# Kernel optimization log

Measured on AMD Instinct MI355X. Metric: run time of the kernel, lower is better.

The kernel has to match this reference:

```python
import jax, jax.numpy as jnp
import numpy as np

B, N, D = 8, 1024, 768
H = 12
HD = D // H
LN_EPS = 1e-5
EPS = 1e-8


def setup_inputs() -> dict:
    key = jax.random.key(0)
    ks = jax.random.split(key, 16)
    s = 0.02
    return {
        "x": jax.random.normal(ks[0], (B, N, D), jnp.float32),
        "low_freq_feat": jax.random.normal(ks[1], (B, N, D), jnp.float32),
        "high_freq_feat": jax.random.normal(ks[2], (B, N, D), jnp.float32),
        "W_qkv_id": jax.random.normal(ks[3], (D, 3 * D), jnp.float32) * s,
        "W_qkv_attr": jax.random.normal(ks[4], (D, 3 * D), jnp.float32) * s,
        "W_fg_id": jax.random.normal(ks[5], (D, D), jnp.float32) * s,
        "b_fg_id": jnp.zeros((D,), jnp.float32),
        "W_fg_attr": jax.random.normal(ks[6], (D, D), jnp.float32) * s,
        "b_fg_attr": jnp.zeros((D,), jnp.float32),
        "W_proj_id": jax.random.normal(ks[7], (D, D), jnp.float32) * s,
        "b_proj_id": jnp.zeros((D,), jnp.float32),
        "W_proj_attr": jax.random.normal(ks[8], (D, D), jnp.float32) * s,
        "b_proj_attr": jnp.zeros((D,), jnp.float32),
        "ln_id_g": jnp.ones((D,), jnp.float32),
        "ln_id_b": jnp.zeros((D,), jnp.float32),
        "ln_attr_g": jnp.ones((D,), jnp.float32),
        "ln_attr_b": jnp.zeros((D,), jnp.float32),
        "ortho_temperature": jnp.float32(1.0),
        "freq_guide_strength": jnp.float32(0.3),
    }


def _layernorm(x, g, b):
    mu = x.mean(-1, keepdims=True)
    var = ((x - mu) ** 2).mean(-1, keepdims=True)
    return (x - mu) * jax.lax.rsqrt(var + LN_EPS) * g + b


def reference(x, low_freq_feat, high_freq_feat,
              W_qkv_id, W_qkv_attr,
              W_fg_id, b_fg_id, W_fg_attr, b_fg_attr,
              W_proj_id, b_proj_id, W_proj_attr, b_proj_attr,
              ln_id_g, ln_id_b, ln_attr_g, ln_attr_b,
              ortho_temperature, freq_guide_strength):
    b, n, d = x.shape
    scale = HD ** -0.5

    def split_qkv(t):
        t = t.reshape(b, n, 3, H, HD).transpose(2, 0, 3, 1, 4)
        return t[0], t[1], t[2]

    q_id, k_id, v_id = split_qkv(x @ W_qkv_id)
    q_at, k_at, v_at = split_qkv(x @ W_qkv_attr)

    fs = jax.nn.sigmoid(freq_guide_strength)
    low_g = (low_freq_feat @ W_fg_id + b_fg_id).reshape(b, n, H, HD).transpose(0, 2, 1, 3)
    high_g = (high_freq_feat @ W_fg_attr + b_fg_attr).reshape(b, n, H, HD).transpose(0, 2, 1, 3)
    v_id = v_id + fs * low_g
    v_at = v_at + fs * high_g

    def soft_attn(q, k):
        a = jnp.clip(jnp.einsum('bhnd,bhmd->bhnm', q, k) * scale, -20.0, 20.0)
        return jax.nn.softmax(a, axis=-1)

    attn_id = soft_attn(q_id, k_id)
    attn_at = soft_attn(q_at, k_at)

    # soft orthogonal mask (same mask for both branches)
    overlap = ((attn_id + EPS) * (attn_at + EPS)).sum(-1, keepdims=True)
    temp = jnp.clip(ortho_temperature, 0.1, 5.0)
    mask = jax.nn.sigmoid(-overlap * temp)

    def mask_renorm(a):
        m = a * mask
        m = m / (m.sum(-1, keepdims=True) + EPS)
        return jnp.where(jnp.isnan(m), jnp.zeros_like(m), m)

    attn_id = mask_renorm(attn_id)
    attn_at = mask_renorm(attn_at)

    def branch_out(a, v, W, bias, g, beta):
        o = jnp.einsum('bhnm,bhmd->bhnd', a, v).transpose(0, 2, 1, 3).reshape(b, n, d)
        return _layernorm(o @ W + bias, g, beta)

    id_features = branch_out(attn_id, v_id, W_proj_id, b_proj_id, ln_id_g, ln_id_b)
    attr_features = branch_out(attn_at, v_at, W_proj_attr, b_proj_attr, ln_attr_g, ln_attr_b)
    return (id_features, attr_features)
```

## Files before the change

### kernel.cpp

```cpp
#include <hip/hip_runtime.h>
#include <stdint.h>


typedef __attribute__((ext_vector_type(8))) _Float16 f16x8;
typedef __attribute__((ext_vector_type(4))) _Float16 f16x4;
typedef __attribute__((ext_vector_type(4))) float    f32x4;

__device__ __forceinline__ void g2l16(const void* g, void* l) {
  __builtin_amdgcn_global_load_lds(
      (const __attribute__((address_space(1))) void*)g,
      (__attribute__((address_space(3))) void*)l, 16, 0, 0);
}

#define BARX()   asm volatile("s_barrier" ::: "memory")
#define WAITV0() asm volatile("s_waitcnt vmcnt(0)" ::: "memory")
#define LGKM0()  asm volatile("s_waitcnt lgkmcnt(0)" ::: "memory")
#define SB0()    __builtin_amdgcn_sched_barrier(0)

#define MFMA12(NB)                                                            \
  __builtin_amdgcn_s_setprio(1);                                              \
  _Pragma("unroll")                                                           \
  for (int mt = 0; mt < 4; mt++)                                              \
    _Pragma("unroll")                                                         \
    for (int i = 0; i < 3; i++)                                               \
      acc[mt][(NB) + i] = SWAP                                                \
          ? __builtin_amdgcn_mfma_f32_16x16x32_f16(b[i], a[mt],               \
                                                   acc[mt][(NB) + i], 0, 0, 0)\
          : __builtin_amdgcn_mfma_f32_16x16x32_f16(a[mt], b[i],               \
                                                   acc[mt][(NB) + i], 0, 0, 0);\
  __builtin_amdgcn_s_setprio(0);

template <bool SWAP>
__device__ __forceinline__ void gemm192(const _Float16* __restrict__ A0,
                                        const _Float16* __restrict__ A1,
                                        const _Float16* __restrict__ B0,
                                        const _Float16* __restrict__ B1,
                                        int nb0, int nb1, int m0, int KT,
                                        _Float16* As, _Float16* Bs,
                                        f32x4 (&acc)[4][6]) {
  const int tid = threadIdx.x;
  const int lane = tid & 63, w = tid >> 6;
  const int wm = (w >> 1) * 64, wn = (w & 1) * 96;
  const int l15 = lane & 15, quad = lane >> 4;
  const int srow = lane >> 2;
  const int scol = ((lane & 3) ^ ((lane >> 3) & 3)) * 8;
  const int rg = (quad ^ ((l15 >> 1) & 3)) * 8;
  const int rdA = (wm + l15) * 32 + rg;
  const int rdB = (wn + l15) * 32 + rg;

  const _Float16* gA0a = A0 + (size_t)(m0 + (w * 2) * 16 + srow) * 768 + scol;
  const _Float16* gA1a = gA0a + (size_t)16 * 768;
  const _Float16* gA0b = A1 + (size_t)(m0 + (w * 2) * 16 + srow) * 768 + scol;
  const _Float16* gA1b = gA0b + (size_t)16 * 768;
  const _Float16* gBa[3]; const _Float16* gBb[3]; int lB[3];
#pragma unroll
  for (int i = 0; i < 3; i++) {
    int j = w * 3 + i, hb = j / 12, cb = j % 12;
    gBa[i] = B0 + (size_t)(nb0 + cb * 16 + srow) * 768 + hb * 32 + scol;
    gBb[i] = B1 + (size_t)(nb1 + cb * 16 + srow) * 768 + hb * 32 + scol;
    lB[i] = hb * 6144 + cb * 512;
  }

  auto stageA = [&](int t) {
    const bool s = t >= 12;
    const int kc = (s ? t - 12 : t) * 64;
    const _Float16* a0 = s ? gA0b : gA0a;
    const _Float16* a1 = s ? gA1b : gA1a;
    _Float16* Ab = As + (t & 1) * 16384 + w * 1024;
    g2l16(a0 + kc,      Ab);
    g2l16(a0 + kc + 32, Ab + 8192);
    g2l16(a1 + kc,      Ab + 512);
    g2l16(a1 + kc + 32, Ab + 8704);
  };
  auto stageB = [&](int t) {
    const bool s = t >= 12;
    const int kc = (s ? t - 12 : t) * 64;
    _Float16* Bb = Bs + (t & 1) * 12288;
#pragma unroll
    for (int i = 0; i < 3; i++) {
      const _Float16* p = s ? gBb[i] : gBa[i];
      g2l16(p + kc, Bb + lB[i]);
    }
  };

#pragma unroll
  for (int mt = 0; mt < 4; mt++)
#pragma unroll
    for (int nt = 0; nt < 6; nt++) acc[mt][nt] = (f32x4){0.f, 0.f, 0.f, 0.f};

  stageA(0); stageB(0);
  WAITV0();
  BARX();

  for (int t = 0; t < KT; t++) {
    const _Float16* as = As + (t & 1) * 16384;
    const _Float16* bs = Bs + (t & 1) * 12288;
    const bool st = (t + 1 < KT);
    f16x8 a[4], b[3];

#pragma unroll
    for (int mt = 0; mt < 4; mt++) a[mt] = *(const f16x8*)(as + rdA + mt * 512);
#pragma unroll
    for (int i = 0; i < 3; i++) b[i] = *(const f16x8*)(bs + rdB + i * 512);
    if (st) stageA(t + 1);
    BARX(); LGKM0(); SB0();
    MFMA12(0);
    SB0();
    BARX();

#pragma unroll
    for (int i = 0; i < 3; i++) b[i] = *(const f16x8*)(bs + rdB + (3 + i) * 512);
    if (st) stageB(t + 1);
    BARX(); LGKM0(); SB0();
    MFMA12(3);
    SB0();
    BARX();

#pragma unroll
    for (int mt = 0; mt < 4; mt++)
      a[mt] = *(const f16x8*)(as + 8192 + rdA + mt * 512);
#pragma unroll
    for (int i = 0; i < 3; i++)
      b[i] = *(const f16x8*)(bs + 6144 + rdB + i * 512);
    BARX(); LGKM0(); SB0();
    MFMA12(0);
    SB0();
    BARX();

#pragma unroll
    for (int i = 0; i < 3; i++)
      b[i] = *(const f16x8*)(bs + 6144 + rdB + (3 + i) * 512);
    BARX(); LGKM0(); SB0();
    MFMA12(3);
    SB0();
    WAITV0();
    BARX();
  }
}

__device__ __forceinline__ void tcast32(const float* __restrict__ src,
                                        _Float16* __restrict__ dst,
                                        int N, int n0, int k0) {
  __shared__ float t[32][33];
  int tr = threadIdx.x >> 5, tc = threadIdx.x & 31;
#pragma unroll
  for (int i = 0; i < 4; i++) {
    int r = tr + i * 8;
    t[r][tc] = src[(size_t)(k0 + r) * N + n0 + tc];
  }
  __syncthreads();
#pragma unroll
  for (int i = 0; i < 4; i++) {
    int r = tr + i * 8;
    dst[(size_t)(n0 + r) * 768 + k0 + tc] = (_Float16)t[tc][r];
  }
}

__global__ __launch_bounds__(256) void k_pre(const float* __restrict__ x,
                                             const float* __restrict__ lo,
                                             const float* __restrict__ hi,
                                             const float* __restrict__ fgs,
                                             const float* __restrict__ Wq0,
                                             const float* __restrict__ Wq1,
                                             const float* __restrict__ W0,
                                             const float* __restrict__ W1,
                                             const float* __restrict__ W2,
                                             const float* __restrict__ W3,
                                             _Float16* __restrict__ x_f,
                                             _Float16* __restrict__ low_f,
                                             _Float16* __restrict__ high_f,
                                             _Float16* __restrict__ Dq,
                                             _Float16* __restrict__ D0,
                                             _Float16* __restrict__ D1,
                                             _Float16* __restrict__ D2,
                                             _Float16* __restrict__ D3) {
  int blk = blockIdx.x;
  if (blk < 18432) {
    float scale = 1.f;
    const float* s; _Float16* d;
    if (blk < 6144)       { s = x;  d = x_f; }
    else if (blk < 12288) { s = lo; d = low_f;  blk -= 6144;
                            scale = 1.f / (1.f + __expf(-fgs[0])); }
    else                  { s = hi; d = high_f; blk -= 12288;
                            scale = 1.f / (1.f + __expf(-fgs[0])); }
    int i = blk * 256 + threadIdx.x;
    float4 v = ((const float4*)s)[i];
    f16x4 o = {(_Float16)(v.x * scale), (_Float16)(v.y * scale),
               (_Float16)(v.z * scale), (_Float16)(v.w * scale)};
    *(f16x4*)(d + (size_t)i * 4) = o;
    return;
  }
  blk -= 18432;
  if (blk < 3456) {
    int half = blk / 1728, rem = blk % 1728;
    int xx = rem % 72, yy = rem / 72;
    tcast32(half ? Wq1 : Wq0, Dq + (size_t)half * 2304 * 768, 2304, xx * 32, yy * 32);
  } else {
    blk -= 3456;
    int q = blk / 576, rem = blk % 576;
    int xx = rem % 24, yy = rem / 24;
    const float* src; _Float16* d;
    if (q == 0)      { src = W0; d = D0; }
    else if (q == 1) { src = W1; d = D1; }
    else if (q == 2) { src = W2; d = D2; }
    else             { src = W3; d = D3; }
    tcast32(src, d, 768, xx * 32, yy * 32);
  }
}

__global__ __launch_bounds__(512, 2) void k_gemm_qkv(const _Float16* __restrict__ x_f,
                                                     const _Float16* __restrict__ low_f,
                                                     const _Float16* __restrict__ high_f,
                                                     const _Float16* __restrict__ wqkvt,
                                                     const _Float16* __restrict__ wfgid,
                                                     const _Float16* __restrict__ wfgat,
                                                     const float* __restrict__ bfg_id,
                                                     const float* __restrict__ bfg_at,
                                                     const float* __restrict__ fgs,
                                                     _Float16* __restrict__ Qb,
                                                     _Float16* __restrict__ Kb,
                                                     _Float16* __restrict__ Vtb) {
  __shared__ alignas(16) _Float16 As[32768], Bs[24576];
  f32x4 acc[4][6];
  int bx = blockIdx.x, br = bx / 12, idx = bx % 12;
  int three = idx >> 2, sub = idx & 3;
  int m0 = blockIdx.y * 256;
  int n0abs = br * 2304 + three * 768 + sub * 192;
  int lane = threadIdx.x & 63, w = threadIdx.x >> 6;
  int wm = (w >> 1) * 64, wn = (w & 1) * 96, l15 = lane & 15, quad = lane >> 4;

  if (three == 2) {
    const _Float16* A1 = br ? high_f : low_f;
    const _Float16* B1 = br ? wfgat : wfgid;
    gemm192<false>(x_f, A1, wqkvt, B1, n0abs, sub * 192, m0, 24, As, Bs, acc);
    float fs = 1.f / (1.f + __expf(-fgs[0]));
    const float* bias = br ? bfg_at : bfg_id;
#pragma unroll
    for (int mt = 0; mt < 4; mt++)
#pragma unroll
      for (int nt = 0; nt < 6; nt++) {
        int c = sub * 192 + wn + nt * 16 + l15;
        int h = c >> 6, hd = c & 63;
        int m = m0 + wm + mt * 16 + quad * 4;
        int b = m >> 10, tok = m & 1023;
        size_t head = (size_t)(br * 96 + b * 12 + h);
        float bv = fs * bias[c];
        f32x4 v = acc[mt][nt];
        f16x4 o;
#pragma unroll
        for (int r = 0; r < 4; r++) o[r] = (_Float16)(v[r] + bv);
        *(f16x4*)(Vtb + (head * 64 + hd) * 1024 + tok) = o;
      }
  } else {
    gemm192<true>(x_f, x_f, wqkvt, wqkvt, n0abs, n0abs, m0, 12, As, Bs, acc);
    float qscl = (three == 0) ? 0.125f * 1.44269504f : 1.0f;
    _Float16* dst = (three == 0) ? Qb : Kb;
#pragma unroll
    for (int mt = 0; mt < 4; mt++)
#pragma unroll
      for (int nt = 0; nt < 6; nt++) {
        int m = m0 + wm + mt * 16 + l15;
        int c = sub * 192 + wn + nt * 16 + quad * 4;
        int h = c >> 6, hd = c & 63;
        int b = m >> 10, tok = m & 1023;
        size_t head = (size_t)(br * 96 + b * 12 + h);
        f32x4 v = acc[mt][nt];
        f16x4 o;
#pragma unroll
        for (int r = 0; r < 4; r++) o[r] = (_Float16)(v[r] * qscl);
        *(f16x4*)(dst + (head * 1024 + tok) * 64 + hd) = o;
      }
  }
}

__global__ __launch_bounds__(256, 3) void k_attn(const _Float16* __restrict__ Qb,
                                                 const _Float16* __restrict__ Kb,
                                                 const _Float16* __restrict__ Vtb,
                                                 _Float16* __restrict__ Ob) {
  __shared__ alignas(16) _Float16 Qs[128 * 64];
  __shared__ alignas(16) _Float16 Ks[128 * 64];
  __shared__ alignas(16) _Float16 Vts[64 * 128];
  int hl = blockIdx.x;
  int br = hl / 96, bh = hl % 96;
  int qbase = blockIdx.y * 128;
  const _Float16* Qh = Qb + (size_t)hl * 65536;
  const _Float16* Kh = Kb + (size_t)hl * 65536;
  const _Float16* Vth = Vtb + (size_t)hl * 65536;
  int lane = threadIdx.x & 63, w = threadIdx.x >> 6;
  int l15 = lane & 15, quad = lane >> 4;
  const int key7 = l15 & 7;

  {
    int rr = lane >> 3, sg = (lane & 7) ^ rr;
#pragma unroll
    for (int i = 0; i < 4; i++) {
      int c = w * 4 + i;
      g2l16(Qh + (size_t)(qbase + c * 8 + rr) * 64 + sg * 8, Qs + c * 512);
    }
  }
  auto stage_kv = [&](int n0) {
    int rr8 = lane >> 3, sg8 = ((lane & 7) ^ rr8) * 8;
    int rr16 = lane >> 4;
#pragma unroll
    for (int i = 0; i < 4; i++) {
      int c = w * 4 + i;
      g2l16(Kh + (size_t)(n0 + c * 8 + rr8) * 64 + sg8, Ks + c * 512);
      int vrow = c * 4 + rr16;
      int sg16 = ((lane & 15) ^ (vrow & 15)) * 8;
      g2l16(Vth + (size_t)vrow * 1024 + n0 + sg16, Vts + c * 512);
    }
  };
  stage_kv(0);

  f32x4 o[2][4];
#pragma unroll
  for (int qg = 0; qg < 2; qg++)
#pragma unroll
    for (int i = 0; i < 4; i++) o[qg][i] = (f32x4){0.f, 0.f, 0.f, 0.f};
  float rs0 = 0.f, rs1 = 0.f;
  f16x8 bq[2][2];
  const f32x4 zero = (f32x4){0.f, 0.f, 0.f, 0.f};
  const int g0 = (quad ^ key7) * 8, g1 = ((4 + quad) ^ key7) * 8;

  for (int kt = 0; kt < 8; kt++) {
    __syncthreads();
    if (kt == 0) {
#pragma unroll
      for (int qg = 0; qg < 2; qg++) {
        bq[qg][0] = *(const f16x8*)(Qs + (w * 32 + qg * 16 + l15) * 64 + g0);
        bq[qg][1] = *(const f16x8*)(Qs + (w * 32 + qg * 16 + l15) * 64 + g1);
      }
    }
    f32x4 c0, c1;
    {
      f16x8 a0 = *(const f16x8*)(Ks + l15 * 64 + g0);
      f16x8 a1 = *(const f16x8*)(Ks + l15 * 64 + g1);
      c0 = __builtin_amdgcn_mfma_f32_16x16x32_f16(a0, bq[0][0], zero, 0, 0, 0);
      c0 = __builtin_amdgcn_mfma_f32_16x16x32_f16(a1, bq[0][1], c0, 0, 0, 0);
      c1 = __builtin_amdgcn_mfma_f32_16x16x32_f16(a0, bq[1][0], zero, 0, 0, 0);
      c1 = __builtin_amdgcn_mfma_f32_16x16x32_f16(a1, bq[1][1], c1, 0, 0, 0);
    }
#pragma unroll
    for (int nt = 0; nt < 8; nt++) {
      f32x4 n0_, n1_;
      if (nt < 7) {
        f16x8 a0 = *(const f16x8*)(Ks + ((nt + 1) * 16 + l15) * 64 + g0);
        f16x8 a1 = *(const f16x8*)(Ks + ((nt + 1) * 16 + l15) * 64 + g1);
        n0_ = __builtin_amdgcn_mfma_f32_16x16x32_f16(a0, bq[0][0], zero, 0, 0, 0);
        n0_ = __builtin_amdgcn_mfma_f32_16x16x32_f16(a1, bq[0][1], n0_, 0, 0, 0);
        n1_ = __builtin_amdgcn_mfma_f32_16x16x32_f16(a0, bq[1][0], zero, 0, 0, 0);
        n1_ = __builtin_amdgcn_mfma_f32_16x16x32_f16(a1, bq[1][1], n1_, 0, 0, 0);
      }
      f16x4 pt0, pt1;
#pragma unroll
      for (int r = 0; r < 4; r++) {
        float p = __builtin_amdgcn_exp2f(c0[r]);
        rs0 += p; pt0[r] = (_Float16)p;
      }
#pragma unroll
      for (int r = 0; r < 4; r++) {
        float p = __builtin_amdgcn_exp2f(c1[r]);
        rs1 += p; pt1[r] = (_Float16)p;
      }
#pragma unroll
      for (int hdt = 0; hdt < 4; hdt++) {
        int g = ((2 * nt + (quad >> 1)) ^ l15) * 8 + (quad & 1) * 4;
        f16x4 av = *(const f16x4*)(Vts + (hdt * 16 + l15) * 128 + g);
        o[0][hdt] = __builtin_amdgcn_mfma_f32_16x16x16f16(av, pt0, o[0][hdt], 0, 0, 0);
        o[1][hdt] = __builtin_amdgcn_mfma_f32_16x16x16f16(av, pt1, o[1][hdt], 0, 0, 0);
      }
      if (nt < 7) { c0 = n0_; c1 = n1_; }
    }
    __syncthreads();
    if (kt < 7) stage_kv((kt + 1) * 128);
  }
  _Float16* Os = Qs;
  int b = bh / 12, h = bh % 12;
#pragma unroll
  for (int qg = 0; qg < 2; qg++) {
    float l = qg ? rs1 : rs0;
    l += __shfl_xor(l, 16);
    l += __shfl_xor(l, 32);
    float inv = 1.f / l;
    int row = w * 32 + qg * 16 + l15;
#pragma unroll
    for (int hdt = 0; hdt < 4; hdt++) {
      f16x4 u;
#pragma unroll
      for (int r = 0; r < 4; r++) u[r] = (_Float16)(o[qg][hdt][r] * inv);
      int G8 = hdt * 2 + (quad >> 1);
      int pos = ((G8 ^ (row & 7)) * 8) + (quad & 1) * 4;
      *(f16x4*)(Os + row * 64 + pos) = u;
    }
  }
  __syncthreads();
  size_t base = ((size_t)br * 8192 + b * 1024 + qbase) * 768 + h * 64;
#pragma unroll
  for (int it = 0; it < 4; it++) {
    int row = it * 32 + w * 8 + (lane >> 3);
    int G8 = lane & 7;
    f16x8 u = *(const f16x8*)(Os + row * 64 + ((G8 ^ (row & 7)) * 8));
    *(f16x8*)(Ob + base + (size_t)row * 768 + G8 * 8) = u;
  }
}

__global__ __launch_bounds__(512, 2) void k_gemm_proj2(const _Float16* __restrict__ Aid,
                                                       const _Float16* __restrict__ Aat,
                                                       const _Float16* __restrict__ Bid,
                                                       const _Float16* __restrict__ Bat,
                                                       _Float16* __restrict__ Yid,
                                                       _Float16* __restrict__ Yat) {
  __shared__ alignas(16) _Float16 As[32768], Bs[24576];
  f32x4 acc[4][6];
  int half = blockIdx.x >> 2;
  int n0 = (blockIdx.x & 3) * 192, m0 = blockIdx.y * 256;
  const _Float16* A = half ? Aat : Aid;
  const _Float16* Bt = half ? Bat : Bid;
  _Float16* Y = half ? Yat : Yid;
  gemm192<true>(A, A, Bt, Bt, n0, n0, m0, 12, As, Bs, acc);
  int lane = threadIdx.x & 63, w = threadIdx.x >> 6;
  int wm = (w >> 1) * 64, wn = (w & 1) * 96, l15 = lane & 15, quad = lane >> 4;
#pragma unroll
  for (int mt = 0; mt < 4; mt++)
#pragma unroll
    for (int nt = 0; nt < 6; nt++) {
      int m = m0 + wm + mt * 16 + l15;
      int n = n0 + wn + nt * 16 + quad * 4;
      f32x4 v = acc[mt][nt];
      f16x4 o;
#pragma unroll
      for (int r = 0; r < 4; r++) o[r] = (_Float16)v[r];
      *(f16x4*)(Y + (size_t)m * 768 + n) = o;
    }
}

__global__ __launch_bounds__(256) void k_ln(const _Float16* __restrict__ Yid,
                                            const _Float16* __restrict__ Yat,
                                            const float* __restrict__ bp_id,
                                            const float* __restrict__ bp_at,
                                            const float* __restrict__ g_id,
                                            const float* __restrict__ be_id,
                                            const float* __restrict__ g_at,
                                            const float* __restrict__ be_at,
                                            float* __restrict__ out) {
  int w = threadIdx.x >> 6, lane = threadIdx.x & 63;
  int r = blockIdx.x * 4 + w;
  int br = r >> 13, m = r & 8191;
  const _Float16* Y = br ? Yat : Yid;
  const float* bp = br ? bp_at : bp_id;
  const float* g = br ? g_at : g_id;
  const float* be = br ? be_at : be_id;
  float v[12], sum = 0.f, sq = 0.f;
#pragma unroll
  for (int j = 0; j < 3; j++) {
    int c = j * 256 + lane * 4;
    f16x4 y = *(const f16x4*)(Y + (size_t)m * 768 + c);
    float4 bv = *(const float4*)(bp + c);
#pragma unroll
    for (int r2 = 0; r2 < 4; r2++) {
      float t = (float)y[r2] + ((const float*)&bv)[r2];
      v[j * 4 + r2] = t; sum += t; sq += t * t;
    }
  }
#pragma unroll
  for (int d = 1; d < 64; d <<= 1) { sum += __shfl_xor(sum, d); sq += __shfl_xor(sq, d); }
  float mu = sum * (1.f / 768.f);
  float var = sq * (1.f / 768.f) - mu * mu;
  float rstd = rsqrtf(var + 1e-5f);
  float* op = out + (size_t)br * 6291456 + (size_t)m * 768;
#pragma unroll
  for (int j = 0; j < 3; j++) {
    int c = j * 256 + lane * 4;
    float4 gv = *(const float4*)(g + c);
    float4 bev = *(const float4*)(be + c);
    float4 ov;
#pragma unroll
    for (int r2 = 0; r2 < 4; r2++)
      ((float*)&ov)[r2] = (v[j * 4 + r2] - mu) * rstd * ((const float*)&gv)[r2] +
                          ((const float*)&bev)[r2];
    *(float4*)(op + c) = ov;
  }
}

extern "C" void kernel_launch(void* const* d_in, const int* in_sizes, int n_in,
                              void* d_out, int out_size, void* d_ws, size_t ws_size,
                              hipStream_t stream) {
  const float* x       = (const float*)d_in[0];
  const float* lowf    = (const float*)d_in[1];
  const float* highf   = (const float*)d_in[2];
  const float* Wqkv_id = (const float*)d_in[3];
  const float* Wqkv_at = (const float*)d_in[4];
  const float* Wfg_id  = (const float*)d_in[5];
  const float* bfg_id  = (const float*)d_in[6];
  const float* Wfg_at  = (const float*)d_in[7];
  const float* bfg_at  = (const float*)d_in[8];
  const float* Wpr_id  = (const float*)d_in[9];
  const float* bpr_id  = (const float*)d_in[10];
  const float* Wpr_at  = (const float*)d_in[11];
  const float* bpr_at  = (const float*)d_in[12];
  const float* g_id    = (const float*)d_in[13];
  const float* be_id   = (const float*)d_in[14];
  const float* g_at    = (const float*)d_in[15];
  const float* be_at   = (const float*)d_in[16];
  const float* fgs     = (const float*)d_in[18];

  char* ws = (char*)d_ws;
  _Float16* x_f    = (_Float16*)(ws + 0);
  _Float16* low_f  = (_Float16*)(ws + 12582912);
  _Float16* high_f = (_Float16*)(ws + 25165824);
  _Float16* wqkvt  = (_Float16*)(ws + 37748736);
  _Float16* wfgidt = (_Float16*)(ws + 44826624);
  _Float16* wfgatt = (_Float16*)(ws + 46006272);
  _Float16* wpridt = (_Float16*)(ws + 47185920);
  _Float16* wpratt = (_Float16*)(ws + 48365568);
  _Float16* Qb     = (_Float16*)(ws + 74711040);
  _Float16* Kb     = (_Float16*)(ws + 99876864);
  _Float16* Vtb    = (_Float16*)(ws + 125042688);
  _Float16* Ob     = (_Float16*)(ws + 150208512);
  _Float16* Y_id   = (_Float16*)(ws + 0);
  _Float16* Y_at   = (_Float16*)(ws + 49545216);

  k_pre<<<24192, 256, 0, stream>>>(x, lowf, highf, fgs,
                                   Wqkv_id, Wqkv_at, Wfg_id, Wfg_at, Wpr_id, Wpr_at,
                                   x_f, low_f, high_f,
                                   wqkvt, wfgidt, wfgatt, wpridt, wpratt);
  k_gemm_qkv<<<dim3(24, 32), 512, 0, stream>>>(x_f, low_f, high_f, wqkvt,
                                               wfgidt, wfgatt, bfg_id, bfg_at, fgs,
                                               Qb, Kb, Vtb);
  k_attn<<<dim3(192, 8), 256, 0, stream>>>(Qb, Kb, Vtb, Ob);
  k_gemm_proj2<<<dim3(8, 32), 512, 0, stream>>>(Ob, Ob + 6291456, wpridt, wpratt,
                                                Y_id, Y_at);
  k_ln<<<4096, 256, 0, stream>>>(Y_id, Y_at, bpr_id, bpr_at, g_id, be_id, g_at, be_at,
                                 (float*)d_out);
}
```

Baseline: 390.7 us.

## Double-buffer K/V tiles in attention kernel and reorder grid for head locality

The attention kernel now keeps two LDS buffers for K and V^T. It issues the global-to-LDS load for the next key tile before computing on the current one, so memory latency overlaps with MFMA work instead of being exposed between syncthreads. The grid is transposed so the eight query blocks of one head are adjacent, which should improve L2 reuse of K/V. LDS use grows from 48KB to 80KB per block, and the occupancy hint drops from 3 to 2 blocks per CU. There is also a possible hazard: the WAR ordering on buffer reuse relies on the end-of-iteration barrier.

```diff
diff --git a/kernel.cpp b/kernel.cpp
--- a/kernel.cpp
+++ b/kernel.cpp
@@ -273,16 +273,16 @@
   }
 }
 
-__global__ __launch_bounds__(256, 3) void k_attn(const _Float16* __restrict__ Qb,
+__global__ __launch_bounds__(256, 2) void k_attn(const _Float16* __restrict__ Qb,
                                                  const _Float16* __restrict__ Kb,
                                                  const _Float16* __restrict__ Vtb,
                                                  _Float16* __restrict__ Ob) {
   __shared__ alignas(16) _Float16 Qs[128 * 64];
-  __shared__ alignas(16) _Float16 Ks[128 * 64];
-  __shared__ alignas(16) _Float16 Vts[64 * 128];
-  int hl = blockIdx.x;
+  __shared__ alignas(16) _Float16 Ks[2][128 * 64];
+  __shared__ alignas(16) _Float16 Vts[2][64 * 128];
+  int hl = blockIdx.y;
   int br = hl / 96, bh = hl % 96;
-  int qbase = blockIdx.y * 128;
+  int qbase = blockIdx.x * 128;
   const _Float16* Qh = Qb + (size_t)hl * 65536;
   const _Float16* Kh = Kb + (size_t)hl * 65536;
   const _Float16* Vth = Vtb + (size_t)hl * 65536;
@@ -290,6 +290,19 @@
   int l15 = lane & 15, quad = lane >> 4;
   const int key7 = l15 & 7;
 
+  auto stage_kv = [&](int n0, int buf) {
+    int rr8 = lane >> 3, sg8 = ((lane & 7) ^ rr8) * 8;
+    int rr16 = lane >> 4;
+#pragma unroll
+    for (int i = 0; i < 4; i++) {
+      int c = w * 4 + i;
+      g2l16(Kh + (size_t)(n0 + c * 8 + rr8) * 64 + sg8, &Ks[buf][0] + c * 512);
+      int vrow = c * 4 + rr16;
+      int sg16 = ((lane & 15) ^ (vrow & 15)) * 8;
+      g2l16(Vth + (size_t)vrow * 1024 + n0 + sg16, &Vts[buf][0] + c * 512);
+    }
+  };
+
   {
     int rr = lane >> 3, sg = (lane & 7) ^ rr;
 #pragma unroll
@@ -298,19 +311,9 @@
       g2l16(Qh + (size_t)(qbase + c * 8 + rr) * 64 + sg * 8, Qs + c * 512);
     }
   }
-  auto stage_kv = [&](int n0) {
-    int rr8 = lane >> 3, sg8 = ((lane & 7) ^ rr8) * 8;
-    int rr16 = lane >> 4;
-#pragma unroll
-    for (int i = 0; i < 4; i++) {
-      int c = w * 4 + i;
-      g2l16(Kh + (size_t)(n0 + c * 8 + rr8) * 64 + sg8, Ks + c * 512);
-      int vrow = c * 4 + rr16;
-      int sg16 = ((lane & 15) ^ (vrow & 15)) * 8;
-      g2l16(Vth + (size_t)vrow * 1024 + n0 + sg16, Vts + c * 512);
-    }
-  };
-  stage_kv(0);
+  stage_kv(0, 0);
+  WAITV0();
+  BARX();
 
   f32x4 o[2][4];
 #pragma unroll
@@ -322,19 +325,21 @@
   const f32x4 zero = (f32x4){0.f, 0.f, 0.f, 0.f};
   const int g0 = (quad ^ key7) * 8, g1 = ((4 + quad) ^ key7) * 8;
 
+#pragma unroll
+  for (int qg = 0; qg < 2; qg++) {
+    bq[qg][0] = *(const f16x8*)(Qs + (w * 32 + qg * 16 + l15) * 64 + g0);
+    bq[qg][1] = *(const f16x8*)(Qs + (w * 32 + qg * 16 + l15) * 64 + g1);
+  }
+
   for (int kt = 0; kt < 8; kt++) {
-    __syncthreads();
-    if (kt == 0) {
-#pragma unroll
-      for (int qg = 0; qg < 2; qg++) {
-        bq[qg][0] = *(const f16x8*)(Qs + (w * 32 + qg * 16 + l15) * 64 + g0);
-        bq[qg][1] = *(const f16x8*)(Qs + (w * 32 + qg * 16 + l15) * 64 + g1);
-      }
-    }
+    if (kt < 7) stage_kv((kt + 1) * 128, (kt + 1) & 1);
+    const _Float16* Kc = &Ks[kt & 1][0];
+    const _Float16* Vc = &Vts[kt & 1][0];
+
     f32x4 c0, c1;
     {
-      f16x8 a0 = *(const f16x8*)(Ks + l15 * 64 + g0);
-      f16x8 a1 = *(const f16x8*)(Ks + l15 * 64 + g1);
+      f16x8 a0 = *(const f16x8*)(Kc + l15 * 64 + g0);
+      f16x8 a1 = *(const f16x8*)(Kc + l15 * 64 + g1);
       c0 = __builtin_amdgcn_mfma_f32_16x16x32_f16(a0, bq[0][0], zero, 0, 0, 0);
       c0 = __builtin_amdgcn_mfma_f32_16x16x32_f16(a1, bq[0][1], c0, 0, 0, 0);
       c1 = __builtin_amdgcn_mfma_f32_16x16x32_f16(a0, bq[1][0], zero, 0, 0, 0);
@@ -344,8 +349,8 @@
     for (int nt = 0; nt < 8; nt++) {
       f32x4 n0_, n1_;
       if (nt < 7) {
-        f16x8 a0 = *(const f16x8*)(Ks + ((nt + 1) * 16 + l15) * 64 + g0);
-        f16x8 a1 = *(const f16x8*)(Ks + ((nt + 1) * 16 + l15) * 64 + g1);
+        f16x8 a0 = *(const f16x8*)(Kc + ((nt + 1) * 16 + l15) * 64 + g0);
+        f16x8 a1 = *(const f16x8*)(Kc + ((nt + 1) * 16 + l15) * 64 + g1);
         n0_ = __builtin_amdgcn_mfma_f32_16x16x32_f16(a0, bq[0][0], zero, 0, 0, 0);
         n0_ = __builtin_amdgcn_mfma_f32_16x16x32_f16(a1, bq[0][1], n0_, 0, 0, 0);
         n1_ = __builtin_amdgcn_mfma_f32_16x16x32_f16(a0, bq[1][0], zero, 0, 0, 0);
@@ -365,14 +370,16 @@
 #pragma unroll
       for (int hdt = 0; hdt < 4; hdt++) {
         int g = ((2 * nt + (quad >> 1)) ^ l15) * 8 + (quad & 1) * 4;
-        f16x4 av = *(const f16x4*)(Vts + (hdt * 16 + l15) * 128 + g);
+        f16x4 av = *(const f16x4*)(Vc + (hdt * 16 + l15) * 128 + g);
         o[0][hdt] = __builtin_amdgcn_mfma_f32_16x16x16f16(av, pt0, o[0][hdt], 0, 0, 0);
         o[1][hdt] = __builtin_amdgcn_mfma_f32_16x16x16f16(av, pt1, o[1][hdt], 0, 0, 0);
       }
       if (nt < 7) { c0 = n0_; c1 = n1_; }
     }
-    __syncthreads();
-    if (kt < 7) stage_kv((kt + 1) * 128);
+    if (kt < 7) {
+      WAITV0();
+      BARX();
+    }
   }
   _Float16* Os = Qs;
   int b = bh / 12, h = bh % 12;
@@ -527,7 +534,7 @@
   k_gemm_qkv<<<dim3(24, 32), 512, 0, stream>>>(x_f, low_f, high_f, wqkvt,
                                                wfgidt, wfgatt, bfg_id, bfg_at, fgs,
                                                Qb, Kb, Vtb);
-  k_attn<<<dim3(192, 8), 256, 0, stream>>>(Qb, Kb, Vtb, Ob);
+  k_attn<<<dim3(8, 192), 256, 0, stream>>>(Qb, Kb, Vtb, Ob);
   k_gemm_proj2<<<dim3(8, 32), 512, 0, stream>>>(Ob, Ob + 6291456, wpridt, wpratt,
                                                 Y_id, Y_at);
   k_ln<<<4096, 256, 0, stream>>>(Y_id, Y_at, bpr_id, bpr_at, g_id, be_id, g_at, be_at,
```

New measurement: 400.3 us. 2.5% more time.
